# Kernel tuning notes

Measured on AMD Instinct MI355X. Metric: run time of the kernel, lower is better.

## Reference

```python
import jax, jax.numpy as jnp
import numpy as np

DIM_VAL = 128
DIM_ATTN = 64

def setup_inputs() -> dict:
    key = jax.random.key(0)
    k_x, k_q, k_k, k_v = jax.random.split(key, 4)
    B, S = 4, 4096
    x = jax.random.normal(k_x, (B, S, DIM_VAL), dtype=jnp.float32)
    # nn.Linear(in, out, bias=False): weight shape [out, in]; y = x @ W^T
    Wq = jax.random.normal(k_q, (DIM_ATTN, DIM_VAL), dtype=jnp.float32) / np.sqrt(DIM_VAL)
    Wk = jax.random.normal(k_k, (DIM_ATTN, DIM_VAL), dtype=jnp.float32) / np.sqrt(DIM_VAL)
    Wv = jax.random.normal(k_v, (DIM_VAL, DIM_VAL), dtype=jnp.float32) / np.sqrt(DIM_VAL)
    return {"x": x, "Wq": Wq, "Wk": Wk, "Wv": Wv}

def reference(x, Wq, Wk, Wv):
    # QKV projections (bias-free linear: x @ W^T)
    Q = jnp.einsum('bsd,ad->bsa', x, Wq)   # [B,S,dim_attn]
    K = jnp.einsum('bsd,ad->bsa', x, Wk)   # [B,S,dim_attn]
    V = jnp.einsum('bsd,vd->bsv', x, Wv)   # [B,S,dim_val]
    scale = 1.0 / jnp.sqrt(jnp.asarray(Q.shape[-1], dtype=Q.dtype))
    scores = jnp.einsum('bqa,bka->bqk', Q, K) * scale  # [B,S,S]
    a = jax.nn.softmax(scores, axis=-1)
    return jnp.einsum('bqk,bkv->bqv', a, V)  # [B,S,dim_val]
```

## Files before the change

kernel.cpp:

```cpp
#include <hip/hip_runtime.h>

typedef _Float16 half8 __attribute__((ext_vector_type(8)));
typedef _Float16 half4v __attribute__((ext_vector_type(4)));
typedef float   float4v __attribute__((ext_vector_type(4)));

#define S_LEN 4096
#define NBATCH 4
#define NCHUNK 4
#define WS_W16 0
#define WS_QH  32768
#define WS_KH  1081344
#define WS_VT  2129920
#define WS_L   4227072

__global__ __launch_bounds__(256) void init_kernel(const float* __restrict__ Wq,
                                                   const float* __restrict__ Wk,
                                                   const float* __restrict__ Wv,
                                                   _Float16* __restrict__ w16,
                                                   float4v* __restrict__ out4,
                                                   float4v* __restrict__ l4) {
    int i = blockIdx.x * 256 + threadIdx.x;
    out4[i] = (float4v){0.f, 0.f, 0.f, 0.f};
    if (i < 4096) l4[i] = (float4v){0.f, 0.f, 0.f, 0.f};
    if (i < 32768) {
        int row = i >> 7, col = i & 127;
        float v;
        if (row < 64)       v = Wq[row * 128 + col];
        else if (row < 128) v = Wk[(row - 64) * 128 + col];
        else                v = Wv[(row - 128) * 128 + col];
        w16[i] = (_Float16)v;
    }
}

__global__ __launch_bounds__(256) void qkv_proj_kernel(const float* __restrict__ x,
                                                       const _Float16* __restrict__ w16,
                                                       _Float16* __restrict__ Qh,
                                                       _Float16* __restrict__ Kh,
                                                       _Float16* __restrict__ Vt) {
    __shared__ _Float16 xs[16 * 136];
    const int t = threadIdx.x;
    const int blk = blockIdx.x;
    const float* xb = x + (size_t)blk * 16 * 128;

    for (int it = 0; it < 2; ++it) {
        int i = t + it * 256;
        int row = i >> 5, c4 = i & 31;
        float4v f = ((const float4v*)xb)[i];
        half4v h;
        h[0] = (_Float16)f[0]; h[1] = (_Float16)f[1];
        h[2] = (_Float16)f[2]; h[3] = (_Float16)f[3];
        *(half4v*)&xs[row * 136 + c4 * 4] = h;
    }
    __syncthreads();

    const int w = t >> 6, lane = t & 63, quad = lane >> 4, n16 = lane & 15;

    half8 a[4];
    for (int c = 0; c < 4; ++c)
        a[c] = *(const half8*)&xs[n16 * 136 + c * 32 + quad * 8];

    float4v acc[4];
    for (int nb = 0; nb < 4; ++nb) acc[nb] = (float4v){0.f, 0.f, 0.f, 0.f};

    for (int c = 0; c < 4; ++c) {
        for (int nb = 0; nb < 4; ++nb) {
            int oc = w * 64 + nb * 16 + n16;
            half8 bfr = *(const half8*)&w16[(size_t)oc * 128 + c * 32 + quad * 8];
            acc[nb] = __builtin_amdgcn_mfma_f32_16x16x32_f16(a[c], bfr, acc[nb], 0, 0, 0);
        }
    }

    const int token0 = blk * 16 + quad * 4;
    if (w == 0) {
        for (int nb = 0; nb < 4; ++nb)
            for (int r = 0; r < 4; ++r)
                Qh[(size_t)(token0 + r) * 64 + nb * 16 + n16] = (_Float16)acc[nb][r];
    } else if (w == 1) {
        for (int nb = 0; nb < 4; ++nb)
            for (int r = 0; r < 4; ++r)
                Kh[(size_t)(token0 + r) * 64 + nb * 16 + n16] = (_Float16)acc[nb][r];
    } else {
        int bb = token0 >> 12, s0 = token0 & 4095;
        for (int nb = 0; nb < 4; ++nb) {
            int vc = (w - 2) * 64 + nb * 16 + n16;
            half4v h;
            h[0] = (_Float16)acc[nb][0]; h[1] = (_Float16)acc[nb][1];
            h[2] = (_Float16)acc[nb][2]; h[3] = (_Float16)acc[nb][3];
            *(half4v*)&Vt[((size_t)bb * 128 + vc) * S_LEN + s0] = h;
        }
    }
}

#define KT 64
__global__ __launch_bounds__(256) void flash_kernel(const _Float16* __restrict__ Qh,
                                                    const _Float16* __restrict__ Kh,
                                                    const _Float16* __restrict__ Vt,
                                                    float* __restrict__ out,
                                                    float* __restrict__ lbuf) {
    __shared__ _Float16 Ks[KT * 72];
    __shared__ _Float16 Vs[128 * 72];

    const int t = threadIdx.x;
    const int qt = blockIdx.x, chunk = blockIdx.y, b = blockIdx.z;
    const int w = t >> 6, lane = t & 63, quad = lane >> 4, n16 = lane & 15;

    const size_t qrowA = (size_t)b * S_LEN + qt * 128 + w * 16 + n16;
    const size_t qrowB = qrowA + 64;
    half8 aQ0A = *(const half8*)&Qh[qrowA * 64 + quad * 8];
    half8 aQ1A = *(const half8*)&Qh[qrowA * 64 + 32 + quad * 8];
    half8 aQ0B = *(const half8*)&Qh[qrowB * 64 + quad * 8];
    half8 aQ1B = *(const half8*)&Qh[qrowB * 64 + 32 + quad * 8];

    float4v OA[8], OB[8];
    for (int vb = 0; vb < 8; ++vb) {
        OA[vb] = (float4v){0.f, 0.f, 0.f, 0.f};
        OB[vb] = (float4v){0.f, 0.f, 0.f, 0.f};
    }
    float lsumA = 0.f, lsumB = 0.f;

    const _Float16* Kb = Kh + (size_t)b * S_LEN * 64;
    const _Float16* Vb = Vt + (size_t)b * 128 * S_LEN;

    const int kt0 = chunk * (S_LEN / KT / NCHUNK);
    const int kt1 = kt0 + (S_LEN / KT / NCHUNK);

    const int kr0 = t >> 3, kc0 = t & 7;
    const int kr1 = (t + 256) >> 3;

    half8 kreg0, kreg1, vreg[4];
    {
        const half8* srcK = (const half8*)(Kb + (size_t)kt0 * KT * 64);
        kreg0 = srcK[t];
        kreg1 = srcK[t + 256];
        for (int it = 0; it < 4; ++it) {
            int i = t + it * 256, row = i >> 3, c8 = i & 7;
            vreg[it] = *(const half8*)&Vb[(size_t)row * S_LEN + kt0 * KT + c8 * 8];
        }
    }

    for (int kt = kt0; kt < kt1; ++kt) {
        __syncthreads();
        *(half8*)&Ks[kr0 * 72 + kc0 * 8] = kreg0;
        *(half8*)&Ks[kr1 * 72 + kc0 * 8] = kreg1;
        for (int it = 0; it < 4; ++it) {
            int i = t + it * 256, row = i >> 3, c8 = i & 7;
            *(half8*)&Vs[row * 72 + c8 * 8] = vreg[it];
        }
        __syncthreads();

        if (kt + 1 < kt1) {
            const half8* srcK = (const half8*)(Kb + (size_t)(kt + 1) * KT * 64);
            kreg0 = srcK[t];
            kreg1 = srcK[t + 256];
            for (int it = 0; it < 4; ++it) {
                int i = t + it * 256, row = i >> 3, c8 = i & 7;
                vreg[it] = *(const half8*)&Vb[(size_t)row * S_LEN + (kt + 1) * KT + c8 * 8];
            }
        }

        half8 aP0A, aP1A, aP0B, aP1B;
        __builtin_amdgcn_s_setprio(1);
#pragma unroll
        for (int nb = 0; nb < 4; ++nb) {
            half8 bK0 = *(const half8*)&Ks[(nb * 16 + n16) * 72 + quad * 8];
            half8 bK1 = *(const half8*)&Ks[(nb * 16 + n16) * 72 + 32 + quad * 8];
            float4v scA = (float4v){0.f, 0.f, 0.f, 0.f};
            float4v scB = (float4v){0.f, 0.f, 0.f, 0.f};
            scA = __builtin_amdgcn_mfma_f32_16x16x32_f16(bK0, aQ0A, scA, 0, 0, 0);
            scA = __builtin_amdgcn_mfma_f32_16x16x32_f16(bK1, aQ1A, scA, 0, 0, 0);
            scB = __builtin_amdgcn_mfma_f32_16x16x32_f16(bK0, aQ0B, scB, 0, 0, 0);
            scB = __builtin_amdgcn_mfma_f32_16x16x32_f16(bK1, aQ1B, scB, 0, 0, 0);
#pragma unroll
            for (int r = 0; r < 4; ++r) {
                float pa = __builtin_amdgcn_exp2f(__builtin_fmaf(scA[r], 0.18033688f, -5.7707802f));
                lsumA += pa;
                float pb = __builtin_amdgcn_exp2f(__builtin_fmaf(scB[r], 0.18033688f, -5.7707802f));
                lsumB += pb;
                int slot = (nb & 1) * 4 + r;
                if (nb < 2) { aP0A[slot] = (_Float16)pa; aP0B[slot] = (_Float16)pb; }
                else        { aP1A[slot] = (_Float16)pa; aP1B[slot] = (_Float16)pb; }
            }
        }
        __builtin_amdgcn_s_setprio(0);

        __builtin_amdgcn_s_setprio(1);
#pragma unroll
        for (int vb = 0; vb < 8; ++vb) {
            const _Float16* vrow = &Vs[(vb * 16 + n16) * 72];
            half4v v00 = *(const half4v*)&vrow[quad * 4];
            half4v v01 = *(const half4v*)&vrow[16 + quad * 4];
            half4v v10 = *(const half4v*)&vrow[32 + quad * 4];
            half4v v11 = *(const half4v*)&vrow[48 + quad * 4];
            half8 bV0, bV1;
#pragma unroll
            for (int j = 0; j < 4; ++j) {
                bV0[j] = v00[j]; bV0[4 + j] = v01[j];
                bV1[j] = v10[j]; bV1[4 + j] = v11[j];
            }
            OA[vb] = __builtin_amdgcn_mfma_f32_16x16x32_f16(aP0A, bV0, OA[vb], 0, 0, 0);
            OA[vb] = __builtin_amdgcn_mfma_f32_16x16x32_f16(aP1A, bV1, OA[vb], 0, 0, 0);
            OB[vb] = __builtin_amdgcn_mfma_f32_16x16x32_f16(aP0B, bV0, OB[vb], 0, 0, 0);
            OB[vb] = __builtin_amdgcn_mfma_f32_16x16x32_f16(aP1B, bV1, OB[vb], 0, 0, 0);
        }
        __builtin_amdgcn_s_setprio(0);
    }

    lsumA += __shfl_xor(lsumA, 16);
    lsumA += __shfl_xor(lsumA, 32);
    lsumB += __shfl_xor(lsumB, 16);
    lsumB += __shfl_xor(lsumB, 32);

    const int rowbaseA = qt * 128 + w * 16;
    const int rowbaseB = rowbaseA + 64;
    if (quad == 0) {
        unsafeAtomicAdd(&lbuf[b * S_LEN + rowbaseA + n16], lsumA);
        unsafeAtomicAdd(&lbuf[b * S_LEN + rowbaseB + n16], lsumB);
    }

    const int row0A = rowbaseA + quad * 4;
    const int row0B = rowbaseB + quad * 4;
    float* obA = out + ((size_t)b * S_LEN + row0A) * 128;
    float* obB = out + ((size_t)b * S_LEN + row0B) * 128;
    for (int vb = 0; vb < 8; ++vb)
        for (int r = 0; r < 4; ++r) {
            unsafeAtomicAdd(&obA[(size_t)r * 128 + vb * 16 + n16], OA[vb][r]);
            unsafeAtomicAdd(&obB[(size_t)r * 128 + vb * 16 + n16], OB[vb][r]);
        }
}

__global__ __launch_bounds__(256) void norm_kernel(float4v* __restrict__ out4,
                                                   const float* __restrict__ lbuf) {
    int i = blockIdx.x * 256 + threadIdx.x;
    float inv = 1.0f / lbuf[i >> 5];
    float4v v = out4[i];
    v[0] *= inv; v[1] *= inv; v[2] *= inv; v[3] *= inv;
    out4[i] = v;
}

extern "C" void kernel_launch(void* const* d_in, const int* in_sizes, int n_in,
                              void* d_out, int out_size, void* d_ws, size_t ws_size,
                              hipStream_t stream) {
    const float* x  = (const float*)d_in[0];
    const float* Wq = (const float*)d_in[1];
    const float* Wk = (const float*)d_in[2];
    const float* Wv = (const float*)d_in[3];
    float* out = (float*)d_out;

    _Float16* ws = (_Float16*)d_ws;
    _Float16* w16 = ws + WS_W16;
    _Float16* Qh  = ws + WS_QH;
    _Float16* Kh  = ws + WS_KH;
    _Float16* Vt  = ws + WS_VT;
    float*    lbuf = (float*)(ws + WS_L);

    init_kernel<<<2048, 256, 0, stream>>>(Wq, Wk, Wv, w16, (float4v*)out, (float4v*)lbuf);
    qkv_proj_kernel<<<NBATCH * S_LEN / 16, 256, 0, stream>>>(x, w16, Qh, Kh, Vt);
    flash_kernel<<<dim3(S_LEN / 128, NCHUNK, NBATCH), 256, 0, stream>>>(Qh, Kh, Vt, out, lbuf);
    norm_kernel<<<2048, 256, 0, stream>>>((float4v*)out, lbuf);
}
```

Baseline: 131.3 us.

## Fuse init and norm into projection and flash kernels, drop LDS staging

Merges the init and normalisation kernels into the projection and flash kernels, cutting four launches to two. The last chunk block for each query tile now normalises that tile, using a global counter to detect it. The flash kernel reads K and a pre-permuted V layout straight from global memory (L1/L2) instead of staging through LDS with syncthreads. The change also doubles the key-split chunks to 8 for more parallelism and converts the weights from fp32 inline. This removes launch and sync overhead but adds redundant global loads, more atomic traffic and a serialised tail normalisation.

```diff
diff --git a/kernel.cpp b/kernel.cpp
--- a/kernel.cpp
+++ b/kernel.cpp
@@ -6,69 +6,66 @@
 
 #define S_LEN 4096
 #define NBATCH 4
-#define NCHUNK 4
-#define WS_W16 0
+#define NCHUNK 8
 #define WS_QH  32768
 #define WS_KH  1081344
 #define WS_VT  2129920
 #define WS_L   4227072
 
-__global__ __launch_bounds__(256) void init_kernel(const float* __restrict__ Wq,
-                                                   const float* __restrict__ Wk,
-                                                   const float* __restrict__ Wv,
-                                                   _Float16* __restrict__ w16,
-                                                   float4v* __restrict__ out4,
-                                                   float4v* __restrict__ l4) {
-    int i = blockIdx.x * 256 + threadIdx.x;
-    out4[i] = (float4v){0.f, 0.f, 0.f, 0.f};
-    if (i < 4096) l4[i] = (float4v){0.f, 0.f, 0.f, 0.f};
-    if (i < 32768) {
-        int row = i >> 7, col = i & 127;
-        float v;
-        if (row < 64)       v = Wq[row * 128 + col];
-        else if (row < 128) v = Wk[(row - 64) * 128 + col];
-        else                v = Wv[(row - 128) * 128 + col];
-        w16[i] = (_Float16)v;
-    }
+static __device__ __forceinline__ half8 cvt8(float4v f0, float4v f1) {
+    half8 h;
+    h[0] = (_Float16)f0[0]; h[1] = (_Float16)f0[1];
+    h[2] = (_Float16)f0[2]; h[3] = (_Float16)f0[3];
+    h[4] = (_Float16)f1[0]; h[5] = (_Float16)f1[1];
+    h[6] = (_Float16)f1[2]; h[7] = (_Float16)f1[3];
+    return h;
 }
 
 __global__ __launch_bounds__(256) void qkv_proj_kernel(const float* __restrict__ x,
-                                                       const _Float16* __restrict__ w16,
+                                                       const float* __restrict__ Wq,
+                                                       const float* __restrict__ Wk,
+                                                       const float* __restrict__ Wv,
                                                        _Float16* __restrict__ Qh,
                                                        _Float16* __restrict__ Kh,
-                                                       _Float16* __restrict__ Vt) {
-    __shared__ _Float16 xs[16 * 136];
-    const int t = threadIdx.x;
-    const int blk = blockIdx.x;
+                                                       _Float16* __restrict__ Vt,
+                                                       float4v* __restrict__ out4,
+                                                       float4v* __restrict__ l4,
+                                                       int* __restrict__ cnt) {
+    const int t = threadIdx.x, blk = blockIdx.x;
+
+    {
+        float4v z = (float4v){0.f, 0.f, 0.f, 0.f};
+        out4[blk * 512 + t]       = z;
+        out4[blk * 512 + 256 + t] = z;
+        if (t < 4) l4[blk * 4 + t] = z;
+        if (blk == 0 && t < 128) cnt[t] = 0;
+    }
+
+    const int w = t >> 6, lane = t & 63, quad = lane >> 4, n16 = lane & 15;
     const float* xb = x + (size_t)blk * 16 * 128;
 
-    for (int it = 0; it < 2; ++it) {
-        int i = t + it * 256;
-        int row = i >> 5, c4 = i & 31;
-        float4v f = ((const float4v*)xb)[i];
-        half4v h;
-        h[0] = (_Float16)f[0]; h[1] = (_Float16)f[1];
-        h[2] = (_Float16)f[2]; h[3] = (_Float16)f[3];
-        *(half4v*)&xs[row * 136 + c4 * 4] = h;
-    }
-    __syncthreads();
-
-    const int w = t >> 6, lane = t & 63, quad = lane >> 4, n16 = lane & 15;
-
     half8 a[4];
+#pragma unroll
+    for (int c = 0; c < 4; ++c) {
+        const float* xr = xb + n16 * 128 + c * 32 + quad * 8;
+        a[c] = cvt8(*(const float4v*)xr, *(const float4v*)(xr + 4));
+    }
+
+    const float* Wsel = (w == 0) ? Wq : (w == 1) ? Wk : Wv;
+    const int rowoff = (w >= 2) ? (w - 2) * 64 : 0;
+
+    float4v acc[4];
+#pragma unroll
+    for (int nb = 0; nb < 4; ++nb) acc[nb] = (float4v){0.f, 0.f, 0.f, 0.f};
+
+#pragma unroll
     for (int c = 0; c < 4; ++c)
-        a[c] = *(const half8*)&xs[n16 * 136 + c * 32 + quad * 8];
-
-    float4v acc[4];
-    for (int nb = 0; nb < 4; ++nb) acc[nb] = (float4v){0.f, 0.f, 0.f, 0.f};
-
-    for (int c = 0; c < 4; ++c) {
+#pragma unroll
         for (int nb = 0; nb < 4; ++nb) {
-            int oc = w * 64 + nb * 16 + n16;
-            half8 bfr = *(const half8*)&w16[(size_t)oc * 128 + c * 32 + quad * 8];
+            const float* wr = Wsel + (size_t)(rowoff + nb * 16 + n16) * 128 + c * 32 + quad * 8;
+            half8 bfr = cvt8(*(const float4v*)wr, *(const float4v*)(wr + 4));
             acc[nb] = __builtin_amdgcn_mfma_f32_16x16x32_f16(a[c], bfr, acc[nb], 0, 0, 0);
         }
-    }
 
     const int token0 = blk * 16 + quad * 4;
     if (w == 0) {
@@ -80,13 +77,17 @@
             for (int r = 0; r < 4; ++r)
                 Kh[(size_t)(token0 + r) * 64 + nb * 16 + n16] = (_Float16)acc[nb][r];
     } else {
-        int bb = token0 >> 12, s0 = token0 & 4095;
+        const int bb = token0 >> 12, s0 = token0 & 4095;
+        const int kt = s0 >> 6, k0 = s0 & 63;
+        const int grp = k0 >> 5, k32 = k0 & 31;
+        const int g = k32 >> 4, q = (k32 >> 2) & 3;
+        const int off = kt * 64 + grp * 32 + q * 8 + g * 4;
         for (int nb = 0; nb < 4; ++nb) {
-            int vc = (w - 2) * 64 + nb * 16 + n16;
+            const int vc = (w - 2) * 64 + nb * 16 + n16;
             half4v h;
             h[0] = (_Float16)acc[nb][0]; h[1] = (_Float16)acc[nb][1];
             h[2] = (_Float16)acc[nb][2]; h[3] = (_Float16)acc[nb][3];
-            *(half4v*)&Vt[((size_t)bb * 128 + vc) * S_LEN + s0] = h;
+            *(half4v*)&Vt[((size_t)bb * 128 + vc) * S_LEN + off] = h;
         }
     }
 }
@@ -96,9 +97,9 @@
                                                     const _Float16* __restrict__ Kh,
                                                     const _Float16* __restrict__ Vt,
                                                     float* __restrict__ out,
-                                                    float* __restrict__ lbuf) {
-    __shared__ _Float16 Ks[KT * 72];
-    __shared__ _Float16 Vs[128 * 72];
+                                                    float* __restrict__ lbuf,
+                                                    int* __restrict__ cnt) {
+    __shared__ int sflag;
 
     const int t = threadIdx.x;
     const int qt = blockIdx.x, chunk = blockIdx.y, b = blockIdx.z;
@@ -112,6 +113,7 @@
     half8 aQ1B = *(const half8*)&Qh[qrowB * 64 + 32 + quad * 8];
 
     float4v OA[8], OB[8];
+#pragma unroll
     for (int vb = 0; vb < 8; ++vb) {
         OA[vb] = (float4v){0.f, 0.f, 0.f, 0.f};
         OB[vb] = (float4v){0.f, 0.f, 0.f, 0.f};
@@ -124,46 +126,15 @@
     const int kt0 = chunk * (S_LEN / KT / NCHUNK);
     const int kt1 = kt0 + (S_LEN / KT / NCHUNK);
 
-    const int kr0 = t >> 3, kc0 = t & 7;
-    const int kr1 = (t + 256) >> 3;
-
-    half8 kreg0, kreg1, vreg[4];
-    {
-        const half8* srcK = (const half8*)(Kb + (size_t)kt0 * KT * 64);
-        kreg0 = srcK[t];
-        kreg1 = srcK[t + 256];
-        for (int it = 0; it < 4; ++it) {
-            int i = t + it * 256, row = i >> 3, c8 = i & 7;
-            vreg[it] = *(const half8*)&Vb[(size_t)row * S_LEN + kt0 * KT + c8 * 8];
-        }
-    }
-
     for (int kt = kt0; kt < kt1; ++kt) {
-        __syncthreads();
-        *(half8*)&Ks[kr0 * 72 + kc0 * 8] = kreg0;
-        *(half8*)&Ks[kr1 * 72 + kc0 * 8] = kreg1;
-        for (int it = 0; it < 4; ++it) {
-            int i = t + it * 256, row = i >> 3, c8 = i & 7;
-            *(half8*)&Vs[row * 72 + c8 * 8] = vreg[it];
-        }
-        __syncthreads();
-
-        if (kt + 1 < kt1) {
-            const half8* srcK = (const half8*)(Kb + (size_t)(kt + 1) * KT * 64);
-            kreg0 = srcK[t];
-            kreg1 = srcK[t + 256];
-            for (int it = 0; it < 4; ++it) {
-                int i = t + it * 256, row = i >> 3, c8 = i & 7;
-                vreg[it] = *(const half8*)&Vb[(size_t)row * S_LEN + (kt + 1) * KT + c8 * 8];
-            }
-        }
+        const _Float16* Ktile = Kb + (size_t)kt * KT * 64;
 
         half8 aP0A, aP1A, aP0B, aP1B;
         __builtin_amdgcn_s_setprio(1);
 #pragma unroll
         for (int nb = 0; nb < 4; ++nb) {
-            half8 bK0 = *(const half8*)&Ks[(nb * 16 + n16) * 72 + quad * 8];
-            half8 bK1 = *(const half8*)&Ks[(nb * 16 + n16) * 72 + 32 + quad * 8];
+            half8 bK0 = *(const half8*)&Ktile[(nb * 16 + n16) * 64 + quad * 8];
+            half8 bK1 = *(const half8*)&Ktile[(nb * 16 + n16) * 64 + 32 + quad * 8];
             float4v scA = (float4v){0.f, 0.f, 0.f, 0.f};
             float4v scB = (float4v){0.f, 0.f, 0.f, 0.f};
             scA = __builtin_amdgcn_mfma_f32_16x16x32_f16(bK0, aQ0A, scA, 0, 0, 0);
@@ -186,17 +157,9 @@
         __builtin_amdgcn_s_setprio(1);
 #pragma unroll
         for (int vb = 0; vb < 8; ++vb) {
-            const _Float16* vrow = &Vs[(vb * 16 + n16) * 72];
-            half4v v00 = *(const half4v*)&vrow[quad * 4];
-            half4v v01 = *(const half4v*)&vrow[16 + quad * 4];
-            half4v v10 = *(const half4v*)&vrow[32 + quad * 4];
-            half4v v11 = *(const half4v*)&vrow[48 + quad * 4];
-            half8 bV0, bV1;
-#pragma unroll
-            for (int j = 0; j < 4; ++j) {
-                bV0[j] = v00[j]; bV0[4 + j] = v01[j];
-                bV1[j] = v10[j]; bV1[4 + j] = v11[j];
-            }
+            const _Float16* vrow = &Vb[(size_t)(vb * 16 + n16) * S_LEN + kt * 64];
+            half8 bV0 = *(const half8*)&vrow[quad * 8];
+            half8 bV1 = *(const half8*)&vrow[32 + quad * 8];
             OA[vb] = __builtin_amdgcn_mfma_f32_16x16x32_f16(aP0A, bV0, OA[vb], 0, 0, 0);
             OA[vb] = __builtin_amdgcn_mfma_f32_16x16x32_f16(aP1A, bV1, OA[vb], 0, 0, 0);
             OB[vb] = __builtin_amdgcn_mfma_f32_16x16x32_f16(aP0B, bV0, OB[vb], 0, 0, 0);
@@ -221,20 +184,32 @@
     const int row0B = rowbaseB + quad * 4;
     float* obA = out + ((size_t)b * S_LEN + row0A) * 128;
     float* obB = out + ((size_t)b * S_LEN + row0B) * 128;
+#pragma unroll
     for (int vb = 0; vb < 8; ++vb)
+#pragma unroll
         for (int r = 0; r < 4; ++r) {
             unsafeAtomicAdd(&obA[(size_t)r * 128 + vb * 16 + n16], OA[vb][r]);
             unsafeAtomicAdd(&obB[(size_t)r * 128 + vb * 16 + n16], OB[vb][r]);
         }
-}
-
-__global__ __launch_bounds__(256) void norm_kernel(float4v* __restrict__ out4,
-                                                   const float* __restrict__ lbuf) {
-    int i = blockIdx.x * 256 + threadIdx.x;
-    float inv = 1.0f / lbuf[i >> 5];
-    float4v v = out4[i];
-    v[0] *= inv; v[1] *= inv; v[2] *= inv; v[3] *= inv;
-    out4[i] = v;
+
+    __threadfence();
+    __syncthreads();
+    if (t == 0) {
+        int old = atomicAdd(&cnt[b * 32 + qt], 1);
+        sflag = (old == NCHUNK - 1);
+    }
+    __syncthreads();
+    if (sflag) {
+        __threadfence();
+        float* ob = out + ((size_t)b * S_LEN + qt * 128) * 128;
+        const float* lb = lbuf + b * S_LEN + qt * 128;
+        for (int i = t; i < 128 * 128; i += 256) {
+            int row = i >> 7;
+            float l = __hip_atomic_load(&lb[row], __ATOMIC_RELAXED, __HIP_MEMORY_SCOPE_AGENT);
+            float v = __hip_atomic_load(&ob[i], __ATOMIC_RELAXED, __HIP_MEMORY_SCOPE_AGENT);
+            ob[i] = v * (1.0f / l);
+        }
+    }
 }
 
 extern "C" void kernel_launch(void* const* d_in, const int* in_sizes, int n_in,
@@ -247,14 +222,13 @@
     float* out = (float*)d_out;
 
     _Float16* ws = (_Float16*)d_ws;
-    _Float16* w16 = ws + WS_W16;
-    _Float16* Qh  = ws + WS_QH;
-    _Float16* Kh  = ws + WS_KH;
-    _Float16* Vt  = ws + WS_VT;
+    int*      cnt  = (int*)d_ws;
+    _Float16* Qh   = ws + WS_QH;
+    _Float16* Kh   = ws + WS_KH;
+    _Float16* Vt   = ws + WS_VT;
     float*    lbuf = (float*)(ws + WS_L);
 
-    init_kernel<<<2048, 256, 0, stream>>>(Wq, Wk, Wv, w16, (float4v*)out, (float4v*)lbuf);
-    qkv_proj_kernel<<<NBATCH * S_LEN / 16, 256, 0, stream>>>(x, w16, Qh, Kh, Vt);
-    flash_kernel<<<dim3(S_LEN / 128, NCHUNK, NBATCH), 256, 0, stream>>>(Qh, Kh, Vt, out, lbuf);
-    norm_kernel<<<2048, 256, 0, stream>>>((float4v*)out, lbuf);
-}
+    qkv_proj_kernel<<<NBATCH * S_LEN / 16, 256, 0, stream>>>(x, Wq, Wk, Wv, Qh, Kh, Vt,
+                                                             (float4v*)out, (float4v*)lbuf, cnt);
+    flash_kernel<<<dim3(S_LEN / 128, NCHUNK, NBATCH), 256, 0, stream>>>(Qh, Kh, Vt, out, lbuf, cnt);
+}
```

After: 291.2 us. 122% more time.
